# Optimization experiments

Measured on AMD Instinct MI355X. Metric: run time of the kernel, lower is better.

Reference implementation:

```python
import jax, jax.numpy as jnp
import numpy as np


def setup_inputs() -> dict:
    key = jax.random.key(0)
    k1, k2, k3 = jax.random.split(key, 3)
    B, C, H, W = 32, 768, 24, 24
    feat1 = jax.random.normal(k1, (B, C, H, W), dtype=jnp.float32)
    feat2 = jax.random.normal(k2, (B, C, H, W), dtype=jnp.float32)
    gamma = jax.random.normal(k3, (1,), dtype=jnp.float32)
    return {"feat1": feat1, "feat2": feat2, "gamma": gamma}


def reference(feat1, feat2, gamma):
    # CMA: channel-wise cross-modal attention over flattened spatial dim.
    B, C, H, W = feat1.shape
    q = feat1.reshape(B, C, H * W)          # [B, C, HW]
    kv = feat2.reshape(B, C, H * W)         # [B, C, HW] (k and v share this)
    attn = jnp.einsum('bcn,bdn->bcd', q, kv)          # [B, C, C] = q @ k^T
    attn = jax.nn.softmax(attn, axis=-1)
    info = jnp.einsum('bcd,bdn->bcn', attn, kv)       # [B, C, HW]
    info = info.reshape(B, C, H, W)
    return gamma[0] * info + feat1
```

## Files before the change

### kernel.cpp

```cpp
#include <hip/hip_runtime.h>

#define B_  32
#define C_  768
#define HW_ 576

#define NCQ 18
#define NCP 24

typedef _Float16 half8 __attribute__((ext_vector_type(8)));
typedef _Float16 half4 __attribute__((ext_vector_type(4)));
typedef float    f32x4 __attribute__((ext_vector_type(4)));

__device__ __forceinline__ void g2l16(const void* g, void* l) {
    __builtin_amdgcn_global_load_lds(
        (const __attribute__((address_space(1))) unsigned int*)g,
        (__attribute__((address_space(3))) unsigned int*)l, 16, 0, 0);
}

#define VM(N) asm volatile("s_waitcnt vmcnt(" #N ")" ::: "memory")


__global__ __launch_bounds__(256) void prep4(const float* __restrict__ f1,
                                             const float* __restrict__ f2,
                                             char* __restrict__ q16,
                                             char* __restrict__ kv16,
                                             char* __restrict__ vt,
                                             int b0, int cur, int nst) {
    __shared__ __align__(16) char Lb[18 * 2064];
    const int bid = blockIdx.x;
    if (bid < nst) {
        const int bz = bid % cur, u = bid / cur;
        const int sel = u & 1, rg = (u >> 1) & 3, ti = u >> 3;
        const float* s = (sel ? f2 : f1) + ((size_t)(b0 + bz) * C_ + ti * 128 + rg * 32) * HW_;
        char* d = (sel ? kv16 : q16) + ((size_t)(bz * 6 + ti)) * (NCQ * 8192) + rg * 2048;

        #pragma unroll
        for (int it = 0; it < 18; ++it) {
            int g     = it * 1024 + threadIdx.x * 4;
            int row_l = g / 576;
            int col   = g - row_l * 576;
            int row   = rg * 32 + row_l;
            int k0    = col >> 5, kk = col & 31;
            int x     = (kk >> 3) ^ ((row >> 1) & 3);
            int loff  = k0 * 2064 + row_l * 64 + x * 16 + (kk & 7) * 2;
            f32x4 v = *(const f32x4*)(s + g);
            half4 h;
            #pragma unroll
            for (int e = 0; e < 4; ++e) h[e] = (_Float16)v[e];
            *(half4*)(Lb + loff) = h;
        }
        __syncthreads();

        #pragma unroll
        for (int p = 0; p < 9; ++p) {
            int idx = p * 256 + threadIdx.x;
            int k0  = idx >> 7;
            int wi  = idx & 127;
            *(f32x4*)(d + (size_t)k0 * 8192 + wi * 16) =
                *(const f32x4*)(Lb + k0 * 2064 + wi * 16);
        }
    } else {
        float* Vsh = (float*)Lb;
        int bid2 = bid - nst;
        const int bz = bid2 % cur, u = bid2 / cur;
        int k0 = u / 3, tj = u % 3;
        int b  = b0 + bz;
        int t  = threadIdx.x;
        #pragma unroll
        for (int p = 0; p < 6; ++p) {
            int fidx = p * 256 + t;
            int dd = fidx / 48, c4 = fidx % 48;
            f32x4 v = *(const f32x4*)(f2 + ((size_t)b * C_ + k0 * 32 + dd) * HW_ + tj * 192 + c4 * 4);
            #pragma unroll
            for (int e = 0; e < 4; ++e) Vsh[dd * 201 + c4 * 4 + e] = v[e];
        }
        __syncthreads();
        char* ob = vt + ((size_t)(bz * 3 + tj) * NCP + k0) * 12288;
        #pragma unroll
        for (int p = 0; p < 3; ++p) {
            int o = p * 256 + t;
            int x = o & 3, n = o >> 2;
            int kc = x ^ ((n >> 1) & 3);
            half8 h;
            #pragma unroll
            for (int j = 0; j < 8; ++j) h[j] = (_Float16)Vsh[(kc * 8 + j) * 201 + n];
            *(half8*)(ob + o * 16) = h;
        }
    }
}

__global__ __launch_bounds__(512, 4) void qk6(const char* __restrict__ q16,
                                              const char* __restrict__ kv16,
                                              _Float16* __restrict__ attnE,
                                              float2* __restrict__ part,
                                              int cur) {
    __shared__ __align__(16) char S[3][24576];
    const int wg = blockIdx.x;
    const int bz = wg % cur, u = wg / cur;
    const int ti = u >> 2, tj = u & 3;
    const int t = threadIdx.x, lane = t & 63, w = t >> 6;
    const int rsub = lane >> 2, cb = (lane & 3) * 16;

    const char *p0, *p1, *p2;
    int o0, o1, o2;
    {
        auto arow = [&](int l) {
            int gr = ti * 192 + 16 * l + rsub;
            return q16 + ((size_t)(bz * 6 + (gr >> 7)) * NCQ) * 8192 + (gr & 127) * 64 + cb;
        };
        auto brow = [&](int l) {
            int gd = tj * 192 + 16 * l + rsub;
            return kv16 + ((size_t)(bz * 6 + (gd >> 7)) * NCQ) * 8192 + (gd & 127) * 64 + cb;
        };
        if (w < 4) {
            p0 = arow(2 * w);     o0 = (2 * w) * 1024;
            p1 = arow(2 * w + 1); o1 = (2 * w + 1) * 1024;
            p2 = brow(8 + w);     o2 = 12288 + (8 + w) * 1024;
        } else {
            int v = w - 4;
            p0 = brow(2 * v);     o0 = 12288 + (2 * v) * 1024;
            p1 = brow(2 * v + 1); o1 = 12288 + (2 * v + 1) * 1024;
            p2 = arow(8 + v);     o2 = (8 + v) * 1024;
        }
    }

    const int wr = (w >> 1) * 48, wc = (w & 1) * 96;
    const int r16 = lane & 15, cg = lane >> 4;
    int offA[3], offB[6];
    #pragma unroll
    for (int m = 0; m < 3; ++m) {
        int ra = wr + m * 16 + r16;
        offA[m] = ra * 64 + ((cg ^ ((ra >> 1) & 3)) << 4);
    }
    #pragma unroll
    for (int n = 0; n < 6; ++n) {
        int rb = wc + n * 16 + r16;
        offB[n] = 12288 + rb * 64 + ((cg ^ ((rb >> 1) & 3)) << 4);
    }

    f32x4 acc[3][6] = {};

#define STG(SLOT) do {                          \
        char* sb_ = &S[SLOT][0];                \
        g2l16(p0, sb_ + o0);                    \
        g2l16(p1, sb_ + o1);                    \
        g2l16(p2, sb_ + o2);                    \
        p0 += 8192; p1 += 8192; p2 += 8192;     \
    } while (0)

    STG(0); STG(1);
    int rd = 0, st = 2;
    for (int c = 0; c < NCQ; ++c) {
        if (c + 2 < NCQ) {
            STG(st); st = (st == 2) ? 0 : st + 1;
            VM(6);
        } else if (c + 2 == NCQ) {
            VM(3);
        } else {
            VM(0);
        }
        __builtin_amdgcn_s_barrier();
        const char* sb = &S[rd][0];
        rd = (rd == 2) ? 0 : rd + 1;
        half8 a0 = *(const half8*)(sb + offA[0]);
        half8 a1 = *(const half8*)(sb + offA[1]);
        half8 a2 = *(const half8*)(sb + offA[2]);
        __builtin_amdgcn_s_setprio(1);
        #pragma unroll
        for (int n = 0; n < 6; ++n) {
            half8 bn = *(const half8*)(sb + offB[n]);
            acc[0][n] = __builtin_amdgcn_mfma_f32_16x16x32_f16(a0, bn, acc[0][n], 0, 0, 0);
            acc[1][n] = __builtin_amdgcn_mfma_f32_16x16x32_f16(a1, bn, acc[1][n], 0, 0, 0);
            acc[2][n] = __builtin_amdgcn_mfma_f32_16x16x32_f16(a2, bn, acc[2][n], 0, 0, 0);
        }
        __builtin_amdgcn_s_setprio(0);
        __builtin_amdgcn_s_barrier();
    }
#undef STG

    const int half = w & 1;
    float mxv[3][4];
    #pragma unroll
    for (int m = 0; m < 3; ++m)
        #pragma unroll
        for (int rg = 0; rg < 4; ++rg) {
            float mx = -1e30f;
            #pragma unroll
            for (int n = 0; n < 6; ++n) mx = fmaxf(mx, acc[m][n][rg]);
            #pragma unroll
            for (int o = 1; o < 16; o <<= 1) mx = fmaxf(mx, __shfl_xor(mx, o));
            mxv[m][rg] = mx;
            float s = 0.f;
            #pragma unroll
            for (int n = 0; n < 6; ++n) s += __expf(acc[m][n][rg] - mx);
            #pragma unroll
            for (int o = 1; o < 16; o <<= 1) s += __shfl_xor(s, o);
            if ((lane & 15) == 0) {
                int row = wr + m * 16 + (lane >> 4) * 4 + rg;
                part[((size_t)bz * C_ + ti * 192 + row) * 8 + tj * 2 + half] =
                    make_float2(mx, s);
            }
        }

    const int col = lane & 15, rbase = (lane >> 4) * 4;
    #pragma unroll
    for (int m = 0; m < 3; ++m)
        #pragma unroll
        for (int n = 0; n < 6; ++n)
            #pragma unroll
            for (int rg = 0; rg < 4; ++rg) {
                int grow = ti * 192 + wr + m * 16 + rbase + rg;
                int gcol = tj * 192 + wc + n * 16 + col;
                attnE[(((size_t)bz * 6 + (grow >> 7)) * NCP + (gcol >> 5)) * 4096
                      + (grow & 127) * 32 + (gcol & 31)] =
                    (_Float16)__expf(acc[m][n][rg] - mxv[m][rg]);
            }
}

__global__ __launch_bounds__(512, 4) void pv11(const _Float16* __restrict__ attnE,
                                               const char* __restrict__ vt,
                                               const float2* __restrict__ part,
                                               const float* __restrict__ gamma,
                                               const float* __restrict__ f1,
                                               float* __restrict__ out,
                                               int b0, int cur) {
    __shared__ __align__(16) char S[4][20480];
    const int wg = blockIdx.x;
    const int bz = wg % cur, u = wg / cur;
    const int ti = u / 3, tj = u % 3;
    const int t = threadIdx.x, lane = t & 63, w = t >> 6;
    const int rsub = lane >> 2, cbb = (lane & 3) * 16;

    const int r0 = t >> 2;
    const int g4 = t & 3;
    const char* srcA = (const char*)(attnE + (((size_t)bz * 6 + ti) * NCP) * 4096) + t * 16;
    const int aw0 = r0 * 64 + ((g4 ^ ((r0 >> 1) & 3)) << 4);

    float2 pm[8];
    float m_row, inv;
    {
        const float2* pr = part + ((size_t)bz * C_ + ti * 128 + r0) * 8;
        #pragma unroll
        for (int i = 0; i < 8; ++i) pm[i] = pr[i];
        float m = pm[0].x;
        #pragma unroll
        for (int i = 1; i < 8; ++i) m = fmaxf(m, pm[i].x);
        float s = 0.f;
        #pragma unroll
        for (int i = 0; i < 8; ++i) s += pm[i].y * __expf(pm[i].x - m);
        m_row = m;
        inv = gamma[0] / s;
    }

    const char* vbase = vt + ((size_t)(bz * 3 + tj) * NCP) * 12288;
    const char *pB0, *pB1;
    int ob0, ob1;
    if (w < 4) {
        pB0 = vbase + (32 * w + rsub) * 64 + cbb;          ob0 = 8192 + (32 * w) * 64;
        pB1 = vbase + (32 * w + 16 + rsub) * 64 + cbb;     ob1 = 8192 + (32 * w + 16) * 64;
    } else {
        pB0 = vbase + (128 + 16 * (w - 4) + rsub) * 64 + cbb;
        ob0 = 8192 + (128 + 16 * (w - 4)) * 64;
        pB1 = vbase; ob1 = 0;
    }

    const int wr = (w >> 2) * 64, wc = (w & 3) * 48;
    const int r16 = lane & 15, cg = lane >> 4;
    int offA[4], offB[3];
    #pragma unroll
    for (int m = 0; m < 4; ++m) {
        int ra = wr + m * 16 + r16;
        offA[m] = ra * 64 + ((cg ^ ((ra >> 1) & 3)) << 4);
    }
    #pragma unroll
    for (int n = 0; n < 3; ++n) {
        int rb = wc + n * 16 + r16;
        offB[n] = 8192 + rb * 64 + ((cg ^ ((rb >> 1) & 3)) << 4);
    }

    f32x4 acc[4][3] = {};
    half8 vaA, vaB;

#define STG_B(SLOT) do {                                  \
        g2l16(pB0, &S[SLOT][0] + ob0); pB0 += 12288;      \
        if (w < 4) { g2l16(pB1, &S[SLOT][0] + ob1); pB1 += 12288; } \
    } while (0)
#define LD_A(V) do { V = *(const half8*)srcA; srcA += 8192; } while (0)
#define WR_A(SLOT, V, H) do {                                          \
        const float fac_ = __expf(pm[H].x - m_row) * inv;              \
        half8 h_;                                                      \
        _Pragma("unroll")                                              \
        for (int e = 0; e < 8; ++e)                                    \
            h_[e] = (_Float16)((float)V[e] * fac_);                    \
        *(half8*)(&S[SLOT][0] + aw0) = h_;                             \
    } while (0)
#define MFMA_SLOT(SB) do {                                             \
        const char* sb_ = (SB);                                        \
        half8 a_[4], b_[3];                                            \
        _Pragma("unroll")                                              \
        for (int m = 0; m < 4; ++m) a_[m] = *(const half8*)(sb_ + offA[m]); \
        _Pragma("unroll")                                              \
        for (int n = 0; n < 3; ++n) b_[n] = *(const half8*)(sb_ + offB[n]); \
        _Pragma("unroll")                                              \
        for (int m = 0; m < 4; ++m)                                    \
            _Pragma("unroll")                                          \
            for (int n = 0; n < 3; ++n)                                \
                acc[m][n] = __builtin_amdgcn_mfma_f32_16x16x32_f16(a_[m], b_[n], acc[m][n], 0, 0, 0); \
    } while (0)

    LD_A(vaA);
    WR_A(0, vaA, 0);
    LD_A(vaB);
    WR_A(1, vaB, 0);
    STG_B(0); STG_B(1);
    LD_A(vaA);
    LD_A(vaB);

    #pragma unroll
    for (int p = 0; p < 12; ++p) {
        const int sa = (2 * p) & 3;
        asm volatile("s_waitcnt lgkmcnt(0)" ::: "memory");
        __builtin_amdgcn_s_barrier();
        if (p < 11) { STG_B((sa + 2) & 3); STG_B((sa + 3) & 3); }
        if (p < 11) { if (w < 4) VM(6); else VM(4); }
        else        { VM(0); }
        __builtin_amdgcn_s_barrier();

        __builtin_amdgcn_s_setprio(1);
        MFMA_SLOT(&S[sa][0]);
        MFMA_SLOT(&S[sa ^ 1][0]);
        __builtin_amdgcn_s_setprio(0);

        if (p < 11) {
            WR_A((sa + 2) & 3, vaA, (2 * p + 2) / 3);
            WR_A((sa + 3) & 3, vaB, (2 * p + 3) / 3);
            if (p < 10) {
                LD_A(vaA);
                LD_A(vaB);
            }
        }
    }
#undef MFMA_SLOT
#undef WR_A
#undef LD_A
#undef STG_B

    const int b = b0 + bz;
    const float* f1b = f1 + ((size_t)b * C_ + ti * 128) * HW_ + tj * 192;
    float*       ob  = out + ((size_t)b * C_ + ti * 128) * HW_ + tj * 192;
    const int col = lane & 15, rbase = (lane >> 4) * 4;
    #pragma unroll
    for (int m = 0; m < 4; ++m)
        #pragma unroll
        for (int n = 0; n < 3; ++n)
            #pragma unroll
            for (int rg = 0; rg < 4; ++rg) {
                int r2 = wr + m * 16 + rbase + rg;
                int c2 = wc + n * 16 + col;
                ob[(size_t)r2 * HW_ + c2] = acc[m][n][rg] + f1b[(size_t)r2 * HW_ + c2];
            }
}

extern "C" void kernel_launch(void* const* d_in, const int* in_sizes, int n_in,
                              void* d_out, int out_size, void* d_ws, size_t ws_size,
                              hipStream_t stream) {
    const float* feat1 = (const float*)d_in[0];
    const float* feat2 = (const float*)d_in[1];
    const float* gamma = (const float*)d_in[2];
    float* out = (float*)d_out;

    const size_t SZ_Q    = (size_t)C_ * HW_ * 2;
    const size_t SZ_ATTN = (size_t)C_ * C_  * 2;
    const size_t SZ_PART = (size_t)C_ * 8 * 8;
    const size_t per_batch = SZ_ATTN + 3 * SZ_Q + SZ_PART;

    int nb = (int)(ws_size / per_batch);
    if (nb < 1) nb = 1;
    if (nb > B_) nb = B_;

    char* ws        = (char*)d_ws;
    _Float16* attnE = (_Float16*)ws;
    char* q16       = ws + (size_t)nb * SZ_ATTN;
    char* kv16      = q16 + (size_t)nb * SZ_Q;
    char* vtb       = kv16 + (size_t)nb * SZ_Q;
    float2* part    = (float2*)(vtb + (size_t)nb * SZ_Q);

    for (int b0 = 0; b0 < B_; b0 += nb) {
        int cur = (B_ - b0 < nb) ? (B_ - b0) : nb;
        prep4<<<cur * 120, 256, 0, stream>>>(feat1, feat2, q16, kv16, vtb, b0, cur, cur * 48);
        qk6<<<cur * 16, 512, 0, stream>>>(q16, kv16, attnE, part, cur);
        pv11<<<cur * 18, 512, 0, stream>>>(attnE, vtb, part, gamma, feat1, out, b0, cur);
    }
}
```

Before: 126.1 us.

## Pipeline prep fp32 loads through LDS ring buffer with async global-to-LDS

```diff
diff --git a/kernel.cpp b/kernel.cpp
--- a/kernel.cpp
+++ b/kernel.cpp
@@ -20,45 +20,57 @@
 #define VM(N) asm volatile("s_waitcnt vmcnt(" #N ")" ::: "memory")
 
 
-__global__ __launch_bounds__(256) void prep4(const float* __restrict__ f1,
+__global__ __launch_bounds__(256) void prep6(const float* __restrict__ f1,
                                              const float* __restrict__ f2,
                                              char* __restrict__ q16,
                                              char* __restrict__ kv16,
                                              char* __restrict__ vt,
                                              int b0, int cur, int nst) {
-    __shared__ __align__(16) char Lb[18 * 2064];
+    __shared__ __align__(16) char Lb[25984];
     const int bid = blockIdx.x;
     if (bid < nst) {
         const int bz = bid % cur, u = bid / cur;
         const int sel = u & 1, rg = (u >> 1) & 3, ti = u >> 3;
         const float* s = (sel ? f2 : f1) + ((size_t)(b0 + bz) * C_ + ti * 128 + rg * 32) * HW_;
-        char* d = (sel ? kv16 : q16) + ((size_t)(bz * 6 + ti)) * (NCQ * 8192) + rg * 2048;
-
-        #pragma unroll
-        for (int it = 0; it < 18; ++it) {
-            int g     = it * 1024 + threadIdx.x * 4;
+        char* d = (sel ? kv16 : q16) + ((size_t)(bz * 6 + ti)) * (NCQ * 8192);
+        const int t = threadIdx.x, lane = t & 63, w = t >> 6;
+        const char* gsrc = (const char*)s + w * 1024 + lane * 16;
+        const int lbase = w * 1024 + lane * 16;
+
+        auto scat = [&](f32x4 v, int g) {
             int row_l = g / 576;
             int col   = g - row_l * 576;
             int row   = rg * 32 + row_l;
             int k0    = col >> 5, kk = col & 31;
             int x     = (kk >> 3) ^ ((row >> 1) & 3);
-            int loff  = k0 * 2064 + row_l * 64 + x * 16 + (kk & 7) * 2;
-            f32x4 v = *(const f32x4*)(s + g);
             half4 h;
             #pragma unroll
             for (int e = 0; e < 4; ++e) h[e] = (_Float16)v[e];
-            *(half4*)(Lb + loff) = h;
-        }
-        __syncthreads();
-
-        #pragma unroll
-        for (int p = 0; p < 9; ++p) {
-            int idx = p * 256 + threadIdx.x;
-            int k0  = idx >> 7;
-            int wi  = idx & 127;
-            *(f32x4*)(d + (size_t)k0 * 8192 + wi * 16) =
-                *(const f32x4*)(Lb + k0 * 2064 + wi * 16);
-        }
+            *(half4*)(d + (size_t)k0 * 8192 + row * 64 + x * 16 + (kk & 7) * 2) = h;
+        };
+
+#define PST(c) do {                                                     \
+        g2l16(gsrc + (size_t)(c) * 8192,        Lb + ((c) % 3) * 8192 + w * 1024); \
+        g2l16(gsrc + (size_t)(c) * 8192 + 4096, Lb + ((c) % 3) * 8192 + 4096 + w * 1024); \
+    } while (0)
+#define PRC(c) do {                                                     \
+        f32x4 v0 = *(const f32x4*)(Lb + ((c) % 3) * 8192 + lbase);      \
+        f32x4 v1 = *(const f32x4*)(Lb + ((c) % 3) * 8192 + 4096 + lbase); \
+        int g0 = (c) * 2048 + w * 256 + lane * 4;                       \
+        scat(v0, g0);                                                   \
+        scat(v1, g0 + 1024);                                            \
+    } while (0)
+
+        PST(0); PST(1);
+        #pragma unroll
+        for (int c = 0; c < 9; ++c) {
+            if (c < 7) { PST(c + 2); VM(4); }
+            else if (c == 7) { VM(2); }
+            else { VM(0); }
+            PRC(c);
+        }
+#undef PRC
+#undef PST
     } else {
         float* Vsh = (float*)Lb;
         int bid2 = bid - nst;
@@ -66,13 +78,19 @@
         int k0 = u / 3, tj = u % 3;
         int b  = b0 + bz;
         int t  = threadIdx.x;
+        f32x4 vv[6];
         #pragma unroll
         for (int p = 0; p < 6; ++p) {
             int fidx = p * 256 + t;
             int dd = fidx / 48, c4 = fidx % 48;
-            f32x4 v = *(const f32x4*)(f2 + ((size_t)b * C_ + k0 * 32 + dd) * HW_ + tj * 192 + c4 * 4);
-            #pragma unroll
-            for (int e = 0; e < 4; ++e) Vsh[dd * 201 + c4 * 4 + e] = v[e];
+            vv[p] = *(const f32x4*)(f2 + ((size_t)b * C_ + k0 * 32 + dd) * HW_ + tj * 192 + c4 * 4);
+        }
+        #pragma unroll
+        for (int p = 0; p < 6; ++p) {
+            int fidx = p * 256 + t;
+            int dd = fidx / 48, c4 = fidx % 48;
+            #pragma unroll
+            for (int e = 0; e < 4; ++e) Vsh[dd * 201 + c4 * 4 + e] = vv[p][e];
         }
         __syncthreads();
         char* ob = vt + ((size_t)(bz * 3 + tj) * NCP + k0) * 12288;
@@ -387,7 +405,7 @@
 
     for (int b0 = 0; b0 < B_; b0 += nb) {
         int cur = (B_ - b0 < nb) ? (B_ - b0) : nb;
-        prep4<<<cur * 120, 256, 0, stream>>>(feat1, feat2, q16, kv16, vtb, b0, cur, cur * 48);
+        prep6<<<cur * 120, 256, 0, stream>>>(feat1, feat2, q16, kv16, vtb, b0, cur, cur * 48);
         qk6<<<cur * 16, 512, 0, stream>>>(q16, kv16, attnE, part, cur);
         pv11<<<cur * 18, 512, 0, stream>>>(attnE, vtb, part, gamma, feat1, out, b0, cur);
     }
```

New measurement: 129.9 us. 3.0% more time.
